# Performance work log

Measured on AMD Instinct MI355X. Metric: run time of the kernel, lower is better.

Reference implementation:

```python
import jax, jax.numpy as jnp
import numpy as np

N = 50000      # nodes
E = 800000     # edges
F_IN = 512     # input feature dim
H1 = 8         # heads layer 1
F_HID = 8      # per-head hidden dim (concat -> 64)
H2 = 1         # heads layer 2
NLAB = 64      # output classes
LRELU_SLOPE = 0.2


def setup_inputs() -> dict:
    key = jax.random.key(0)
    ks = jax.random.split(key, 9)
    inputs = jax.random.normal(ks[0], (N, F_IN), jnp.float32)
    src = jax.random.randint(ks[1], (E,), 0, N, dtype=jnp.int32)
    dst = jax.random.randint(ks[2], (E,), 0, N, dtype=jnp.int32)
    s1 = 1.0 / np.sqrt(F_IN)
    s2 = 1.0 / np.sqrt(H1 * F_HID)
    W1 = jax.random.normal(ks[3], (H1, F_IN, F_HID), jnp.float32) * s1
    a1_src = jax.random.normal(ks[4], (H1, F_HID), jnp.float32) * 0.1
    a1_dst = jax.random.normal(ks[5], (H1, F_HID), jnp.float32) * 0.1
    W2 = jax.random.normal(ks[6], (H2, H1 * F_HID, NLAB), jnp.float32) * s2
    a2_src = jax.random.normal(ks[7], (H2, NLAB), jnp.float32) * 0.1
    a2_dst = jax.random.normal(ks[8], (H2, NLAB), jnp.float32) * 0.1
    return {"inputs": inputs, "W1": W1, "a1_src": a1_src, "a1_dst": a1_dst,
            "W2": W2, "a2_src": a2_src, "a2_dst": a2_dst, "src": src, "dst": dst}


def gat_layer(x, W, a_s, a_d, src, dst):
    # x: [N, F]; W: [H, F, O]; a_s/a_d: [H, O]
    Wh = jnp.einsum('nf,hfo->nho', x, W)                    # [N, H, O]
    es = jnp.einsum('nho,ho->nh', Wh, a_s)                  # [N, H]
    ed = jnp.einsum('nho,ho->nh', Wh, a_d)                  # [N, H]
    e = jax.nn.leaky_relu(es[src] + ed[dst], LRELU_SLOPE)   # [E, H]
    # neighborhood softmax over incoming edges of each dst node
    m = jax.lax.stop_gradient(jax.ops.segment_max(e, dst, num_segments=N))
    ex = jnp.exp(e - m[dst])                                # [E, H]
    den = jax.ops.segment_sum(ex, dst, num_segments=N)      # [N, H]
    alpha = ex / (den[dst] + 1e-10)                         # [E, H]
    msgs = alpha[:, :, None] * Wh[src]                      # [E, H, O]
    return jax.ops.segment_sum(msgs, dst, num_segments=N)   # [N, H, O]


def reference(inputs, W1, a1_src, a1_dst, W2, a2_src, a2_dst, src, dst):
    # eval mode: dropout rate 0, identity
    h = gat_layer(inputs, W1, a1_src, a1_dst, src, dst)     # [N, H1, F_HID]
    h = jax.nn.elu(h.reshape(N, H1 * F_HID))                # concat heads (reduction=False)
    o = gat_layer(h, W2, a2_src, a2_dst, src, dst)          # [N, H2, NLAB]
    o = o.mean(axis=1)                                      # average heads (reduction=True)
    return jax.nn.softmax(o, axis=-1)                       # [N, NLAB] (squeezed)
```

## Files before the change

### kernel.cpp

```cpp
#include <hip/hip_runtime.h>
#include <math.h>

#define N_NODES 50000
#define N_EDGES 800000
#define F_IN    512
#define H1      8
#define F_HID   8
#define C1      64
#define NLAB    64
#define SLOPE   0.2f
#define MAXDEG  64

#define NBIN    98
#define BINCAP  9216
#define NBLK_WT  128
#define NBLK_E   196
#define NBLK_G1  782

typedef __attribute__((ext_vector_type(8))) short short8;
typedef __attribute__((ext_vector_type(4))) float f32x4;

__device__ __forceinline__ float bf_lo(unsigned u) { return __uint_as_float(u << 16); }
__device__ __forceinline__ float bf_hi(unsigned u) { return __uint_as_float(u & 0xFFFF0000u); }
__device__ __forceinline__ unsigned short f2bf(float x) {
    unsigned bits = __float_as_uint(x);
    return (unsigned short)((bits + 0x7FFF + ((bits >> 16) & 1)) >> 16);
}

__global__ void k_prep(const float* __restrict__ W1, unsigned short* __restrict__ Bh,
                       unsigned short* __restrict__ Bl) {
    int i = blockIdx.x * 256 + threadIdx.x;
    int c = i >> 9, f = i & 511;
    float v = W1[(c >> 3) * (F_IN * F_HID) + f * F_HID + (c & 7)];
    unsigned bits = __float_as_uint(v);
    float r = v - __uint_as_float(bits & 0xFFFF0000u);
    Bh[i] = (unsigned short)(bits >> 16);
    Bl[i] = (unsigned short)(__float_as_uint(r) >> 16);
}

__launch_bounds__(256, 4)
__global__ void k_gemm1b(const float* __restrict__ X, const unsigned short* __restrict__ Bh,
                         const unsigned short* __restrict__ Bl, const float* __restrict__ a_s,
                         const float* __restrict__ a_d, float* __restrict__ es1,
                         unsigned short* __restrict__ wh1, float* __restrict__ ed,
                         const int* __restrict__ src, const int* __restrict__ dst,
                         int2* __restrict__ ebuf, int* __restrict__ gctr) {
    __shared__ unsigned short sBh[64][136];
    __shared__ unsigned short sBl[64][136];

    const int b = blockIdx.x;
    const int t = threadIdx.x;
    if (b < NBLK_E) {
        int* hist = (int*)&sBh[0][0];
        int* cur  = hist + 128;
        if (t < NBIN) hist[t] = 0;
        __syncthreads();
        int4 dv[4], sv[4];
        const int e0 = b * 4096 + t * 4;
        #pragma unroll
        for (int i = 0; i < 4; i++) {
            int e = e0 + i * 1024;
            if (e < N_EDGES) {
                dv[i] = *(const int4*)(dst + e);
                sv[i] = *(const int4*)(src + e);
                atomicAdd(&hist[dv[i].x >> 9], 1);
                atomicAdd(&hist[dv[i].y >> 9], 1);
                atomicAdd(&hist[dv[i].z >> 9], 1);
                atomicAdd(&hist[dv[i].w >> 9], 1);
            }
        }
        __syncthreads();
        if (t < NBIN) cur[t] = atomicAdd(&gctr[t], hist[t]);
        __syncthreads();
        #pragma unroll
        for (int i = 0; i < 4; i++) {
            int e = e0 + i * 1024;
            if (e < N_EDGES) {
                int d, s, sl;
                d = dv[i].x; s = sv[i].x; sl = atomicAdd(&cur[d >> 9], 1);
                ebuf[(size_t)(d >> 9) * BINCAP + min(sl, BINCAP - 1)] = make_int2(d, s);
                d = dv[i].y; s = sv[i].y; sl = atomicAdd(&cur[d >> 9], 1);
                ebuf[(size_t)(d >> 9) * BINCAP + min(sl, BINCAP - 1)] = make_int2(d, s);
                d = dv[i].z; s = sv[i].z; sl = atomicAdd(&cur[d >> 9], 1);
                ebuf[(size_t)(d >> 9) * BINCAP + min(sl, BINCAP - 1)] = make_int2(d, s);
                d = dv[i].w; s = sv[i].w; sl = atomicAdd(&cur[d >> 9], 1);
                ebuf[(size_t)(d >> 9) * BINCAP + min(sl, BINCAP - 1)] = make_int2(d, s);
            }
        }
        return;
    }

    const int lane = t & 63, w = t >> 6;
    const int r0 = (b - NBLK_E) * 64 + w * 16;
    const int m = lane & 15, quad = lane >> 4;
    int row = r0 + m; if (row >= N_NODES) row = N_NODES - 1;
    const float* xrow = X + (size_t)row * F_IN + quad * 8;

    const int sc = t >> 2;
    const int sp = t & 3;

    f32x4 acc[4] = {};
    float4 pxa[4], pxb[4];
    #pragma unroll
    for (int i = 0; i < 4; i++) {
        pxa[i] = *(const float4*)(xrow + i * 32);
        pxb[i] = *(const float4*)(xrow + i * 32 + 4);
    }

    for (int chunk = 0; chunk < 4; chunk++) {
        const int k0 = chunk * 128;
        if (chunk) __syncthreads();
        #pragma unroll
        for (int i = 0; i < 4; i++) {
            *(short8*)(&sBh[sc][sp * 32 + i * 8]) =
                *(const short8*)(Bh + sc * F_IN + k0 + sp * 32 + i * 8);
            *(short8*)(&sBl[sc][sp * 32 + i * 8]) =
                *(const short8*)(Bl + sc * F_IN + k0 + sp * 32 + i * 8);
        }
        __syncthreads();
        #pragma unroll
        for (int i = 0; i < 4; i++) {
            float xs[8] = {pxa[i].x, pxa[i].y, pxa[i].z, pxa[i].w,
                           pxb[i].x, pxb[i].y, pxb[i].z, pxb[i].w};
            if (chunk < 3) {
                const int ktn = k0 + 128 + i * 32;
                pxa[i] = *(const float4*)(xrow + ktn);
                pxb[i] = *(const float4*)(xrow + ktn + 4);
            }
            short8 ah, al;
            #pragma unroll
            for (int j = 0; j < 8; j++) {
                unsigned bits = __float_as_uint(xs[j]);
                float rr = xs[j] - __uint_as_float(bits & 0xFFFF0000u);
                ah[j] = (short)(bits >> 16);
                al[j] = (short)(__float_as_uint(rr) >> 16);
            }
            #pragma unroll
            for (int s = 0; s < 4; s++) {
                short8 bh = *(const short8*)(&sBh[s * 16 + m][i * 32 + quad * 8]);
                short8 bl = *(const short8*)(&sBl[s * 16 + m][i * 32 + quad * 8]);
                acc[s] = __builtin_amdgcn_mfma_f32_16x16x32_bf16(al, bh, acc[s], 0, 0, 0);
                acc[s] = __builtin_amdgcn_mfma_f32_16x16x32_bf16(ah, bl, acc[s], 0, 0, 0);
                acc[s] = __builtin_amdgcn_mfma_f32_16x16x32_bf16(ah, bh, acc[s], 0, 0, 0);
            }
        }
    }
    __syncthreads();
    unsigned short* sWh = &sBh[0][0] + w * 1024;
    #pragma unroll
    for (int s = 0; s < 4; s++)
        #pragma unroll
        for (int reg = 0; reg < 4; reg++)
            sWh[(quad * 4 + reg) * 64 + s * 16 + m] = f2bf(acc[s][reg]);
    __syncthreads();
    const int rr = lane & 15, p = lane >> 4;
    const int n = r0 + rr;
    if (n >= N_NODES) return;
    float es2v[2], edv[2];
    #pragma unroll
    for (int hh = 0; hh < 2; hh++) {
        int h = 2 * p + hh;
        float s = 0.f, dsum = 0.f;
        #pragma unroll
        for (int j = 0; j < 8; j++) {
            float v = __uint_as_float((unsigned)sWh[rr * 64 + h * 8 + j] << 16);
            s += v * a_s[h * 8 + j];
            dsum += v * a_d[h * 8 + j];
        }
        es2v[hh] = s; edv[hh] = dsum;
    }
    *(float2*)(es1 + n * 8 + 2 * p) = make_float2(es2v[0], es2v[1]);
    *(short8*)(wh1 + (size_t)n * 64 + p * 16)     = *(const short8*)(sWh + rr * 64 + p * 16);
    *(short8*)(wh1 + (size_t)n * 64 + p * 16 + 8) = *(const short8*)(sWh + rr * 64 + p * 16 + 8);
    *(float2*)(ed + n * 8 + 2 * p) = make_float2(edv[0], edv[1]);
}

__global__ void k_csr(const int2* __restrict__ ebuf, const int* __restrict__ gctr,
                      int* __restrict__ deg, int* __restrict__ colPad) {
    __shared__ int cnt[512];
    const int b = blockIdx.x, t = threadIdx.x;
    const int lo = b << 9;
    const int cnum = min(gctr[b], BINCAP);
    for (int i = t; i < 512; i += 256) cnt[i] = 0;
    __syncthreads();
    const int2* eb2 = ebuf + (size_t)b * BINCAP;
    for (int i = t; i < cnum; i += 256) {
        int2 e = eb2[i];
        int sl = atomicAdd(&cnt[e.x - lo], 1);
        colPad[(e.x << 6) | min(sl, MAXDEG - 1)] = e.y;
    }
    __syncthreads();
    for (int i = t; i < 512; i += 256) {
        int n = lo + i;
        if (n < N_NODES) deg[n] = min(cnt[i], MAXDEG);
    }
}

__launch_bounds__(256)
__global__ void k_agg1g2(const float* __restrict__ es1, const unsigned short* __restrict__ wh1,
                         const float* __restrict__ ed,
                         const int* __restrict__ deg, const int* __restrict__ colPad,
                         const float* __restrict__ W2, const float* __restrict__ a2s,
                         const float* __restrict__ a2d,
                         float* __restrict__ es2, unsigned short* __restrict__ wh2,
                         float* __restrict__ ed2) {
    __shared__ float Ws[64 * 64];
    __shared__ float hs[32][64];
    __shared__ int scol[32][68];
    const int t = threadIdx.x;
    #pragma unroll
    for (int i = 0; i < 4; i++) {
        int flat = i * 256 + t;
        *(float4*)(Ws + flat * 4) = *(const float4*)(W2 + flat * 4);
    }
    const int n0 = blockIdx.x * 32;
    for (int i = t; i < 512; i += 256) {
        size_t gi = (size_t)n0 * 16 + i;
        int4 v = (gi < (size_t)N_NODES * 16) ? ((const int4*)colPad)[gi]
                                             : make_int4(0, 0, 0, 0);
        *(int4*)&scol[i >> 4][(i & 15) * 4] = v;
    }
    __syncthreads();

    const int nl = t >> 3, q = t & 7;
    const int n = n0 + nl;
    float o[8] = {};
    if (n < N_NODES) {
        const int d = deg[n];
        const float edq = ed[n * 8 + q];
        float den = 0.f;
        float acc[8] = {};
        #pragma unroll 4
        for (int e = 0; e < d; ++e) {
            int sv = scol[nl][e];
            float x = es1[sv * 8 + q] + edq;
            uint4 u = *(const uint4*)(wh1 + (size_t)sv * 64 + q * 8);
            x = x > 0.f ? x : SLOPE * x;
            float wg = __expf(x);
            den += wg;
            acc[0] += wg * bf_lo(u.x); acc[1] += wg * bf_hi(u.x);
            acc[2] += wg * bf_lo(u.y); acc[3] += wg * bf_hi(u.y);
            acc[4] += wg * bf_lo(u.z); acc[5] += wg * bf_hi(u.z);
            acc[6] += wg * bf_lo(u.w); acc[7] += wg * bf_hi(u.w);
        }
        float inv = 1.f / (den + 1e-10f);
        #pragma unroll
        for (int j = 0; j < 8; j++) {
            float v = acc[j] * inv;
            o[j] = v > 0.f ? v : expm1f(v);
        }
    }
    float4* hp = (float4*)(&hs[nl][q * 8]);
    hp[0] = make_float4(o[0], o[1], o[2], o[3]);
    hp[1] = make_float4(o[4], o[5], o[6], o[7]);
    __syncthreads();

    const int wv = t >> 6, lane = t & 63;
    float as = a2s[lane], ad = a2d[lane];
    #pragma unroll
    for (int j = 0; j < 8; j++) {
        int nn = n0 + wv * 8 + j;
        if (nn >= N_NODES) break;
        float acc = 0.f;
        #pragma unroll
        for (int k = 0; k < 64; k++) acc += hs[wv * 8 + j][k] * Ws[k * 64 + lane];
        wh2[(size_t)nn * 64 + lane] = f2bf(acc);
        float s = acc * as;
        float dd = acc * ad;
        #pragma unroll
        for (int off = 1; off < 64; off <<= 1) {
            s += __shfl_xor(s, off);
            dd += __shfl_xor(dd, off);
        }
        if (lane == 0) { es2[nn] = s; ed2[nn] = dd; }
    }
}

__launch_bounds__(256)
__global__ void k_agg2(const float* __restrict__ es2, const unsigned short* __restrict__ wh2,
                       const float* __restrict__ ed2,
                       const int* __restrict__ deg, const int* __restrict__ colPad,
                       float* __restrict__ out) {
    __shared__ int scol[32][68];
    const int t = threadIdx.x;
    const int n0 = blockIdx.x * 32;
    for (int i = t; i < 512; i += 256) {
        size_t gi = (size_t)n0 * 16 + i;
        int4 v = (gi < (size_t)N_NODES * 16) ? ((const int4*)colPad)[gi]
                                             : make_int4(0, 0, 0, 0);
        *(int4*)&scol[i >> 4][(i & 15) * 4] = v;
    }
    __syncthreads();

    const int nl = t >> 3, q = t & 7;
    const int n = n0 + nl;
    if (n >= N_NODES) return;
    const int d = deg[n];
    const float edn = ed2[n];

    float den = 0.f;
    float acc[8] = {};
    #pragma unroll 4
    for (int e = 0; e < d; ++e) {
        int sv = scol[nl][e];
        float x = es2[sv] + edn;
        uint4 u = *(const uint4*)(wh2 + (size_t)sv * 64 + q * 8);
        x = x > 0.f ? x : SLOPE * x;
        float wg = __expf(x);
        den += wg;
        acc[0] += wg * bf_lo(u.x); acc[1] += wg * bf_hi(u.x);
        acc[2] += wg * bf_lo(u.y); acc[3] += wg * bf_hi(u.y);
        acc[4] += wg * bf_lo(u.z); acc[5] += wg * bf_hi(u.z);
        acc[6] += wg * bf_lo(u.w); acc[7] += wg * bf_hi(u.w);
    }
    float inv = 1.f / (den + 1e-10f);
    float o[8];
    #pragma unroll
    for (int j = 0; j < 8; j++) o[j] = acc[j] * inv;
    float mx = o[0];
    #pragma unroll
    for (int j = 1; j < 8; j++) mx = fmaxf(mx, o[j]);
    mx = fmaxf(mx, __shfl_xor(mx, 1));
    mx = fmaxf(mx, __shfl_xor(mx, 2));
    mx = fmaxf(mx, __shfl_xor(mx, 4));
    float e8[8], sm = 0.f;
    #pragma unroll
    for (int j = 0; j < 8; j++) { e8[j] = __expf(o[j] - mx); sm += e8[j]; }
    sm += __shfl_xor(sm, 1);
    sm += __shfl_xor(sm, 2);
    sm += __shfl_xor(sm, 4);
    float inv2 = 1.f / sm;
    float4* op = (float4*)(out + (size_t)n * 64 + q * 8);
    op[0] = make_float4(e8[0] * inv2, e8[1] * inv2, e8[2] * inv2, e8[3] * inv2);
    op[1] = make_float4(e8[4] * inv2, e8[5] * inv2, e8[6] * inv2, e8[7] * inv2);
}

extern "C" void kernel_launch(void* const* d_in, const int* in_sizes, int n_in,
                              void* d_out, int out_size, void* d_ws, size_t ws_size,
                              hipStream_t stream) {
    const float* X   = (const float*)d_in[0];
    const float* W1  = (const float*)d_in[1];
    const float* a1s = (const float*)d_in[2];
    const float* a1d = (const float*)d_in[3];
    const float* W2  = (const float*)d_in[4];
    const float* a2s = (const float*)d_in[5];
    const float* a2d = (const float*)d_in[6];
    const int*   src = (const int*)d_in[7];
    const int*   dst = (const int*)d_in[8];
    float* out = (float*)d_out;

    char* w = (char*)d_ws;
    size_t off = 0;
    auto alloc = [&](size_t bytes) {
        void* p = w + off;
        off += (bytes + 255) & ~(size_t)255;
        return p;
    };
    unsigned short* Bh   = (unsigned short*)alloc((size_t)C1 * F_IN * 2);
    unsigned short* Bl   = (unsigned short*)alloc((size_t)C1 * F_IN * 2);
    float*          es1  = (float*)alloc((size_t)N_NODES * 8 * 4);
    unsigned short* wh1  = (unsigned short*)alloc((size_t)N_NODES * 64 * 2);
    float*          es2  = (float*)alloc((size_t)N_NODES * 4);
    unsigned short* wh2  = (unsigned short*)alloc((size_t)N_NODES * 64 * 2);
    float*          ed1  = (float*)alloc((size_t)N_NODES * 8 * 4);
    float*          ed2  = (float*)alloc((size_t)N_NODES * 4);
    int*            deg  = (int*)alloc((size_t)N_NODES * 4);
    int*            colPad = (int*)alloc((size_t)N_NODES * MAXDEG * 4);
    int2*           ebuf = (int2*)alloc((size_t)NBIN * BINCAP * 8);
    int*            gctr = (int*)alloc((size_t)NBIN * 4);

    hipMemsetAsync(gctr, 0, NBIN * 4, stream);

    k_prep<<<NBLK_WT, 256, 0, stream>>>(W1, Bh, Bl);
    k_gemm1b<<<NBLK_E + NBLK_G1, 256, 0, stream>>>(X, Bh, Bl, a1s, a1d, es1, wh1, ed1,
                                                   src, dst, ebuf, gctr);
    k_csr<<<NBIN, 256, 0, stream>>>(ebuf, gctr, deg, colPad);
    k_agg1g2<<<(N_NODES + 31) / 32, 256, 0, stream>>>(es1, wh1, ed1, deg, colPad,
                                                      W2, a2s, a2d, es2, wh2, ed2);
    k_agg2<<<(N_NODES + 31) / 32, 256, 0, stream>>>(es2, wh2, ed2, deg, colPad, out);
}
```

Before: 257.8 us.

## Fuse all GAT phases into one cooperative persistent kernel with grid syncs

```diff
diff --git a/kernel.cpp b/kernel.cpp
--- a/kernel.cpp
+++ b/kernel.cpp
@@ -1,5 +1,8 @@
 #include <hip/hip_runtime.h>
+#include <hip/hip_cooperative_groups.h>
 #include <math.h>
+
+namespace cg = cooperative_groups;
 
 #define N_NODES 50000
 #define N_EDGES 800000
@@ -16,6 +19,8 @@
 #define NBLK_WT  128
 #define NBLK_E   196
 #define NBLK_G1  782
+#define NCHUNK  1563
+#define SMEMSZ  34816
 
 typedef __attribute__((ext_vector_type(8))) short short8;
 typedef __attribute__((ext_vector_type(4))) float f32x4;
@@ -27,9 +32,11 @@
     return (unsigned short)((bits + 0x7FFF + ((bits >> 16) & 1)) >> 16);
 }
 
-__global__ void k_prep(const float* __restrict__ W1, unsigned short* __restrict__ Bh,
-                       unsigned short* __restrict__ Bl) {
-    int i = blockIdx.x * 256 + threadIdx.x;
+
+__device__ __forceinline__ void ph_w1split(int task, int t, const float* __restrict__ W1,
+                                           unsigned short* __restrict__ Bh,
+                                           unsigned short* __restrict__ Bl) {
+    int i = task * 256 + t;
     int c = i >> 9, f = i & 511;
     float v = W1[(c >> 3) * (F_IN * F_HID) + f * F_HID + (c & 7)];
     unsigned bits = __float_as_uint(v);
@@ -38,64 +45,80 @@
     Bl[i] = (unsigned short)(__float_as_uint(r) >> 16);
 }
 
-__launch_bounds__(256, 4)
-__global__ void k_gemm1b(const float* __restrict__ X, const unsigned short* __restrict__ Bh,
-                         const unsigned short* __restrict__ Bl, const float* __restrict__ a_s,
-                         const float* __restrict__ a_d, float* __restrict__ es1,
-                         unsigned short* __restrict__ wh1, float* __restrict__ ed,
-                         const int* __restrict__ src, const int* __restrict__ dst,
-                         int2* __restrict__ ebuf, int* __restrict__ gctr) {
-    __shared__ unsigned short sBh[64][136];
-    __shared__ unsigned short sBl[64][136];
-
-    const int b = blockIdx.x;
-    const int t = threadIdx.x;
-    if (b < NBLK_E) {
-        int* hist = (int*)&sBh[0][0];
-        int* cur  = hist + 128;
-        if (t < NBIN) hist[t] = 0;
-        __syncthreads();
-        int4 dv[4], sv[4];
-        const int e0 = b * 4096 + t * 4;
-        #pragma unroll
-        for (int i = 0; i < 4; i++) {
-            int e = e0 + i * 1024;
-            if (e < N_EDGES) {
-                dv[i] = *(const int4*)(dst + e);
-                sv[i] = *(const int4*)(src + e);
-                atomicAdd(&hist[dv[i].x >> 9], 1);
-                atomicAdd(&hist[dv[i].y >> 9], 1);
-                atomicAdd(&hist[dv[i].z >> 9], 1);
-                atomicAdd(&hist[dv[i].w >> 9], 1);
-            }
-        }
-        __syncthreads();
-        if (t < NBIN) cur[t] = atomicAdd(&gctr[t], hist[t]);
-        __syncthreads();
-        #pragma unroll
-        for (int i = 0; i < 4; i++) {
-            int e = e0 + i * 1024;
-            if (e < N_EDGES) {
-                int d, s, sl;
-                d = dv[i].x; s = sv[i].x; sl = atomicAdd(&cur[d >> 9], 1);
-                ebuf[(size_t)(d >> 9) * BINCAP + min(sl, BINCAP - 1)] = make_int2(d, s);
-                d = dv[i].y; s = sv[i].y; sl = atomicAdd(&cur[d >> 9], 1);
-                ebuf[(size_t)(d >> 9) * BINCAP + min(sl, BINCAP - 1)] = make_int2(d, s);
-                d = dv[i].z; s = sv[i].z; sl = atomicAdd(&cur[d >> 9], 1);
-                ebuf[(size_t)(d >> 9) * BINCAP + min(sl, BINCAP - 1)] = make_int2(d, s);
-                d = dv[i].w; s = sv[i].w; sl = atomicAdd(&cur[d >> 9], 1);
-                ebuf[(size_t)(d >> 9) * BINCAP + min(sl, BINCAP - 1)] = make_int2(d, s);
-            }
-        }
-        return;
-    }
-
+__device__ __forceinline__ void ph_bin(int task, int t, char* smem,
+                                       const int* __restrict__ src, const int* __restrict__ dst,
+                                       int2* __restrict__ ebuf, int* __restrict__ gctr) {
+    int* hist = (int*)smem;
+    int* cur  = hist + 128;
+    if (t < NBIN) hist[t] = 0;
+    __syncthreads();
+    int4 dv[4], sv[4];
+    const int e0 = task * 4096 + t * 4;
+    #pragma unroll
+    for (int i = 0; i < 4; i++) {
+        int e = e0 + i * 1024;
+        if (e < N_EDGES) {
+            dv[i] = *(const int4*)(dst + e);
+            sv[i] = *(const int4*)(src + e);
+            atomicAdd(&hist[dv[i].x >> 9], 1);
+            atomicAdd(&hist[dv[i].y >> 9], 1);
+            atomicAdd(&hist[dv[i].z >> 9], 1);
+            atomicAdd(&hist[dv[i].w >> 9], 1);
+        }
+    }
+    __syncthreads();
+    if (t < NBIN) cur[t] = atomicAdd(&gctr[t], hist[t]);
+    __syncthreads();
+    #pragma unroll
+    for (int i = 0; i < 4; i++) {
+        int e = e0 + i * 1024;
+        if (e < N_EDGES) {
+            int d, s, sl;
+            d = dv[i].x; s = sv[i].x; sl = atomicAdd(&cur[d >> 9], 1);
+            ebuf[(size_t)(d >> 9) * BINCAP + min(sl, BINCAP - 1)] = make_int2(d, s);
+            d = dv[i].y; s = sv[i].y; sl = atomicAdd(&cur[d >> 9], 1);
+            ebuf[(size_t)(d >> 9) * BINCAP + min(sl, BINCAP - 1)] = make_int2(d, s);
+            d = dv[i].z; s = sv[i].z; sl = atomicAdd(&cur[d >> 9], 1);
+            ebuf[(size_t)(d >> 9) * BINCAP + min(sl, BINCAP - 1)] = make_int2(d, s);
+            d = dv[i].w; s = sv[i].w; sl = atomicAdd(&cur[d >> 9], 1);
+            ebuf[(size_t)(d >> 9) * BINCAP + min(sl, BINCAP - 1)] = make_int2(d, s);
+        }
+    }
+}
+
+__device__ __forceinline__ void ph_csr(int b, int t, char* smem,
+                                       const int2* __restrict__ ebuf, const int* __restrict__ gctr,
+                                       int* __restrict__ deg, int* __restrict__ colPad) {
+    int* cnt = (int*)smem;
+    const int lo = b << 9;
+    const int cnum = min(gctr[b], BINCAP);
+    for (int i = t; i < 512; i += 256) cnt[i] = 0;
+    __syncthreads();
+    const int2* eb2 = ebuf + (size_t)b * BINCAP;
+    for (int i = t; i < cnum; i += 256) {
+        int2 e = eb2[i];
+        int sl = atomicAdd(&cnt[e.x - lo], 1);
+        colPad[(e.x << 6) | min(sl, MAXDEG - 1)] = e.y;
+    }
+    __syncthreads();
+    for (int i = t; i < 512; i += 256) {
+        int n = lo + i;
+        if (n < N_NODES) deg[n] = min(cnt[i], MAXDEG);
+    }
+}
+
+__device__ __forceinline__ void ph_gemm1(int g, int t, char* smem,
+        const float* __restrict__ X, const unsigned short* __restrict__ Bh,
+        const unsigned short* __restrict__ Bl, const float* __restrict__ a1s,
+        const float* __restrict__ a1d, float* __restrict__ es1,
+        unsigned short* __restrict__ wh1, float* __restrict__ ed1) {
+    unsigned short (*sBh)[136] = (unsigned short(*)[136])smem;
+    unsigned short (*sBl)[136] = (unsigned short(*)[136])(smem + 17408);
     const int lane = t & 63, w = t >> 6;
-    const int r0 = (b - NBLK_E) * 64 + w * 16;
+    const int r0 = g * 64 + w * 16;
     const int m = lane & 15, quad = lane >> 4;
     int row = r0 + m; if (row >= N_NODES) row = N_NODES - 1;
     const float* xrow = X + (size_t)row * F_IN + quad * 8;
-
     const int sc = t >> 2;
     const int sp = t & 3;
 
@@ -106,7 +129,6 @@
         pxa[i] = *(const float4*)(xrow + i * 32);
         pxb[i] = *(const float4*)(xrow + i * 32 + 4);
     }
-
     for (int chunk = 0; chunk < 4; chunk++) {
         const int k0 = chunk * 128;
         if (chunk) __syncthreads();
@@ -146,7 +168,7 @@
         }
     }
     __syncthreads();
-    unsigned short* sWh = &sBh[0][0] + w * 1024;
+    unsigned short* sWh = (unsigned short*)smem + w * 1024;
     #pragma unroll
     for (int s = 0; s < 4; s++)
         #pragma unroll
@@ -164,56 +186,24 @@
         #pragma unroll
         for (int j = 0; j < 8; j++) {
             float v = __uint_as_float((unsigned)sWh[rr * 64 + h * 8 + j] << 16);
-            s += v * a_s[h * 8 + j];
-            dsum += v * a_d[h * 8 + j];
+            s += v * a1s[h * 8 + j];
+            dsum += v * a1d[h * 8 + j];
         }
         es2v[hh] = s; edv[hh] = dsum;
     }
     *(float2*)(es1 + n * 8 + 2 * p) = make_float2(es2v[0], es2v[1]);
     *(short8*)(wh1 + (size_t)n * 64 + p * 16)     = *(const short8*)(sWh + rr * 64 + p * 16);
     *(short8*)(wh1 + (size_t)n * 64 + p * 16 + 8) = *(const short8*)(sWh + rr * 64 + p * 16 + 8);
-    *(float2*)(ed + n * 8 + 2 * p) = make_float2(edv[0], edv[1]);
-}
-
-__global__ void k_csr(const int2* __restrict__ ebuf, const int* __restrict__ gctr,
-                      int* __restrict__ deg, int* __restrict__ colPad) {
-    __shared__ int cnt[512];
-    const int b = blockIdx.x, t = threadIdx.x;
-    const int lo = b << 9;
-    const int cnum = min(gctr[b], BINCAP);
-    for (int i = t; i < 512; i += 256) cnt[i] = 0;
-    __syncthreads();
-    const int2* eb2 = ebuf + (size_t)b * BINCAP;
-    for (int i = t; i < cnum; i += 256) {
-        int2 e = eb2[i];
-        int sl = atomicAdd(&cnt[e.x - lo], 1);
-        colPad[(e.x << 6) | min(sl, MAXDEG - 1)] = e.y;
-    }
-    __syncthreads();
-    for (int i = t; i < 512; i += 256) {
-        int n = lo + i;
-        if (n < N_NODES) deg[n] = min(cnt[i], MAXDEG);
-    }
-}
-
-__launch_bounds__(256)
-__global__ void k_agg1g2(const float* __restrict__ es1, const unsigned short* __restrict__ wh1,
-                         const float* __restrict__ ed,
-                         const int* __restrict__ deg, const int* __restrict__ colPad,
-                         const float* __restrict__ W2, const float* __restrict__ a2s,
-                         const float* __restrict__ a2d,
-                         float* __restrict__ es2, unsigned short* __restrict__ wh2,
-                         float* __restrict__ ed2) {
-    __shared__ float Ws[64 * 64];
-    __shared__ float hs[32][64];
-    __shared__ int scol[32][68];
-    const int t = threadIdx.x;
-    #pragma unroll
-    for (int i = 0; i < 4; i++) {
-        int flat = i * 256 + t;
-        *(float4*)(Ws + flat * 4) = *(const float4*)(W2 + flat * 4);
-    }
-    const int n0 = blockIdx.x * 32;
+    *(float2*)(ed1 + n * 8 + 2 * p) = make_float2(edv[0], edv[1]);
+}
+
+__device__ __forceinline__ void ph_aggC(int n0, int t, const float* Ws, float (*hs)[64],
+        int (*scol)[68],
+        const float* __restrict__ es1, const unsigned short* __restrict__ wh1,
+        const float* __restrict__ ed1, const int* __restrict__ deg,
+        const int* __restrict__ colPad, const float* __restrict__ a2s,
+        const float* __restrict__ a2d, float* __restrict__ es2,
+        unsigned short* __restrict__ wh2, float* __restrict__ ed2) {
     for (int i = t; i < 512; i += 256) {
         size_t gi = (size_t)n0 * 16 + i;
         int4 v = (gi < (size_t)N_NODES * 16) ? ((const int4*)colPad)[gi]
@@ -221,13 +211,12 @@
         *(int4*)&scol[i >> 4][(i & 15) * 4] = v;
     }
     __syncthreads();
-
     const int nl = t >> 3, q = t & 7;
     const int n = n0 + nl;
     float o[8] = {};
     if (n < N_NODES) {
         const int d = deg[n];
-        const float edq = ed[n * 8 + q];
+        const float edq = ed1[n * 8 + q];
         float den = 0.f;
         float acc[8] = {};
         #pragma unroll 4
@@ -254,19 +243,18 @@
     hp[0] = make_float4(o[0], o[1], o[2], o[3]);
     hp[1] = make_float4(o[4], o[5], o[6], o[7]);
     __syncthreads();
-
     const int wv = t >> 6, lane = t & 63;
-    float as = a2s[lane], ad = a2d[lane];
+    const float as = a2s[lane], ad = a2d[lane];
     #pragma unroll
     for (int j = 0; j < 8; j++) {
         int nn = n0 + wv * 8 + j;
         if (nn >= N_NODES) break;
-        float acc = 0.f;
-        #pragma unroll
-        for (int k = 0; k < 64; k++) acc += hs[wv * 8 + j][k] * Ws[k * 64 + lane];
-        wh2[(size_t)nn * 64 + lane] = f2bf(acc);
-        float s = acc * as;
-        float dd = acc * ad;
+        float accv = 0.f;
+        #pragma unroll
+        for (int k = 0; k < 64; k++) accv += hs[wv * 8 + j][k] * Ws[k * 64 + lane];
+        wh2[(size_t)nn * 64 + lane] = f2bf(accv);
+        float s = accv * as;
+        float dd = accv * ad;
         #pragma unroll
         for (int off = 1; off < 64; off <<= 1) {
             s += __shfl_xor(s, off);
@@ -274,16 +262,13 @@
         }
         if (lane == 0) { es2[nn] = s; ed2[nn] = dd; }
     }
-}
-
-__launch_bounds__(256)
-__global__ void k_agg2(const float* __restrict__ es2, const unsigned short* __restrict__ wh2,
-                       const float* __restrict__ ed2,
-                       const int* __restrict__ deg, const int* __restrict__ colPad,
-                       float* __restrict__ out) {
-    __shared__ int scol[32][68];
-    const int t = threadIdx.x;
-    const int n0 = blockIdx.x * 32;
+    __syncthreads();
+}
+
+__device__ __forceinline__ void ph_aggD(int n0, int t, int (*scol)[68],
+        const float* __restrict__ es2, const unsigned short* __restrict__ wh2,
+        const float* __restrict__ ed2, const int* __restrict__ deg,
+        const int* __restrict__ colPad, float* __restrict__ out) {
     for (int i = t; i < 512; i += 256) {
         size_t gi = (size_t)n0 * 16 + i;
         int4 v = (gi < (size_t)N_NODES * 16) ? ((const int4*)colPad)[gi]
@@ -291,48 +276,169 @@
         *(int4*)&scol[i >> 4][(i & 15) * 4] = v;
     }
     __syncthreads();
-
     const int nl = t >> 3, q = t & 7;
     const int n = n0 + nl;
-    if (n >= N_NODES) return;
-    const int d = deg[n];
-    const float edn = ed2[n];
-
-    float den = 0.f;
-    float acc[8] = {};
-    #pragma unroll 4
-    for (int e = 0; e < d; ++e) {
-        int sv = scol[nl][e];
-        float x = es2[sv] + edn;
-        uint4 u = *(const uint4*)(wh2 + (size_t)sv * 64 + q * 8);
-        x = x > 0.f ? x : SLOPE * x;
-        float wg = __expf(x);
-        den += wg;
-        acc[0] += wg * bf_lo(u.x); acc[1] += wg * bf_hi(u.x);
-        acc[2] += wg * bf_lo(u.y); acc[3] += wg * bf_hi(u.y);
-        acc[4] += wg * bf_lo(u.z); acc[5] += wg * bf_hi(u.z);
-        acc[6] += wg * bf_lo(u.w); acc[7] += wg * bf_hi(u.w);
-    }
-    float inv = 1.f / (den + 1e-10f);
-    float o[8];
-    #pragma unroll
-    for (int j = 0; j < 8; j++) o[j] = acc[j] * inv;
-    float mx = o[0];
-    #pragma unroll
-    for (int j = 1; j < 8; j++) mx = fmaxf(mx, o[j]);
-    mx = fmaxf(mx, __shfl_xor(mx, 1));
-    mx = fmaxf(mx, __shfl_xor(mx, 2));
-    mx = fmaxf(mx, __shfl_xor(mx, 4));
-    float e8[8], sm = 0.f;
-    #pragma unroll
-    for (int j = 0; j < 8; j++) { e8[j] = __expf(o[j] - mx); sm += e8[j]; }
-    sm += __shfl_xor(sm, 1);
-    sm += __shfl_xor(sm, 2);
-    sm += __shfl_xor(sm, 4);
-    float inv2 = 1.f / sm;
-    float4* op = (float4*)(out + (size_t)n * 64 + q * 8);
-    op[0] = make_float4(e8[0] * inv2, e8[1] * inv2, e8[2] * inv2, e8[3] * inv2);
-    op[1] = make_float4(e8[4] * inv2, e8[5] * inv2, e8[6] * inv2, e8[7] * inv2);
+    if (n < N_NODES) {
+        const int d = deg[n];
+        const float edn = ed2[n];
+        float den = 0.f;
+        float acc[8] = {};
+        #pragma unroll 4
+        for (int e = 0; e < d; ++e) {
+            int sv = scol[nl][e];
+            float x = es2[sv] + edn;
+            uint4 u = *(const uint4*)(wh2 + (size_t)sv * 64 + q * 8);
+            x = x > 0.f ? x : SLOPE * x;
+            float wg = __expf(x);
+            den += wg;
+            acc[0] += wg * bf_lo(u.x); acc[1] += wg * bf_hi(u.x);
+            acc[2] += wg * bf_lo(u.y); acc[3] += wg * bf_hi(u.y);
+            acc[4] += wg * bf_lo(u.z); acc[5] += wg * bf_hi(u.z);
+            acc[6] += wg * bf_lo(u.w); acc[7] += wg * bf_hi(u.w);
+        }
+        float inv = 1.f / (den + 1e-10f);
+        float o[8];
+        #pragma unroll
+        for (int j = 0; j < 8; j++) o[j] = acc[j] * inv;
+        float mx = o[0];
+        #pragma unroll
+        for (int j = 1; j < 8; j++) mx = fmaxf(mx, o[j]);
+        mx = fmaxf(mx, __shfl_xor(mx, 1));
+        mx = fmaxf(mx, __shfl_xor(mx, 2));
+        mx = fmaxf(mx, __shfl_xor(mx, 4));
+        float e8[8], sm = 0.f;
+        #pragma unroll
+        for (int j = 0; j < 8; j++) { e8[j] = __expf(o[j] - mx); sm += e8[j]; }
+        sm += __shfl_xor(sm, 1);
+        sm += __shfl_xor(sm, 2);
+        sm += __shfl_xor(sm, 4);
+        float inv2 = 1.f / sm;
+        float4* op = (float4*)(out + (size_t)n * 64 + q * 8);
+        op[0] = make_float4(e8[0] * inv2, e8[1] * inv2, e8[2] * inv2, e8[3] * inv2);
+        op[1] = make_float4(e8[4] * inv2, e8[5] * inv2, e8[6] * inv2, e8[7] * inv2);
+    }
+    __syncthreads();
+}
+
+__launch_bounds__(256, 4)
+__global__ void k_mega(const float* __restrict__ X, const float* __restrict__ W1,
+                       const float* __restrict__ a1s, const float* __restrict__ a1d,
+                       const float* __restrict__ W2, const float* __restrict__ a2s,
+                       const float* __restrict__ a2d,
+                       const int* __restrict__ src, const int* __restrict__ dst,
+                       unsigned short* __restrict__ Bh, unsigned short* __restrict__ Bl,
+                       float* __restrict__ es1, unsigned short* __restrict__ wh1,
+                       float* __restrict__ ed1,
+                       float* __restrict__ es2, unsigned short* __restrict__ wh2,
+                       float* __restrict__ ed2,
+                       int* __restrict__ deg, int* __restrict__ colPad,
+                       int2* __restrict__ ebuf, int* __restrict__ gctr,
+                       float* __restrict__ out) {
+    __shared__ __align__(16) char smem[SMEMSZ];
+    __shared__ int sChunk;
+    cg::grid_group grid = cg::this_grid();
+    const int t = threadIdx.x;
+    const int nblk = gridDim.x;
+    int* wctrC = gctr + NBIN;
+    int* wctrD = gctr + NBIN + 1;
+
+    for (int task = blockIdx.x; task < NBLK_WT + NBLK_E; task += nblk) {
+        if (task < NBLK_WT) ph_w1split(task, t, W1, Bh, Bl);
+        else ph_bin(task - NBLK_WT, t, smem, src, dst, ebuf, gctr);
+        __syncthreads();
+    }
+    __threadfence();
+    grid.sync();
+
+    for (int task = blockIdx.x; task < NBIN + NBLK_G1; task += nblk) {
+        if (task < NBIN) ph_csr(task, t, smem, ebuf, gctr, deg, colPad);
+        else ph_gemm1(task - NBIN, t, smem, X, Bh, Bl, a1s, a1d, es1, wh1, ed1);
+        __syncthreads();
+    }
+    __threadfence();
+    grid.sync();
+
+    {
+        float* Ws = (float*)smem;
+        float (*hs)[64] = (float(*)[64])(smem + 16384);
+        int (*scol)[68] = (int(*)[68])(smem + 24576);
+        #pragma unroll
+        for (int i = 0; i < 4; i++) {
+            int flat = i * 256 + t;
+            *(float4*)(Ws + flat * 4) = *(const float4*)(W2 + flat * 4);
+        }
+        while (true) {
+            if (t == 0) sChunk = atomicAdd(wctrC, 1);
+            __syncthreads();
+            const int c = sChunk;
+            if (c >= NCHUNK) break;
+            ph_aggC(c * 32, t, Ws, hs, scol, es1, wh1, ed1, deg, colPad,
+                    a2s, a2d, es2, wh2, ed2);
+        }
+    }
+    __threadfence();
+    grid.sync();
+
+    {
+        int (*scol)[68] = (int(*)[68])smem;
+        while (true) {
+            if (t == 0) sChunk = atomicAdd(wctrD, 1);
+            __syncthreads();
+            const int c = sChunk;
+            if (c >= NCHUNK) break;
+            ph_aggD(c * 32, t, scol, es2, wh2, ed2, deg, colPad, out);
+        }
+    }
+}
+
+__global__ void k_phA(const float* __restrict__ W1, unsigned short* __restrict__ Bh,
+                      unsigned short* __restrict__ Bl, const int* __restrict__ src,
+                      const int* __restrict__ dst, int2* __restrict__ ebuf,
+                      int* __restrict__ gctr) {
+    __shared__ __align__(16) char smem[1024];
+    if (blockIdx.x < NBLK_WT) ph_w1split(blockIdx.x, threadIdx.x, W1, Bh, Bl);
+    else ph_bin(blockIdx.x - NBLK_WT, threadIdx.x, smem, src, dst, ebuf, gctr);
+}
+
+__launch_bounds__(256, 4)
+__global__ void k_phB(const float* __restrict__ X, const unsigned short* __restrict__ Bh,
+                      const unsigned short* __restrict__ Bl, const float* __restrict__ a1s,
+                      const float* __restrict__ a1d, float* __restrict__ es1,
+                      unsigned short* __restrict__ wh1, float* __restrict__ ed1,
+                      const int2* __restrict__ ebuf, const int* __restrict__ gctr,
+                      int* __restrict__ deg, int* __restrict__ colPad) {
+    __shared__ __align__(16) char smem[SMEMSZ];
+    if (blockIdx.x < NBIN) ph_csr(blockIdx.x, threadIdx.x, smem, ebuf, gctr, deg, colPad);
+    else ph_gemm1(blockIdx.x - NBIN, threadIdx.x, smem, X, Bh, Bl, a1s, a1d, es1, wh1, ed1);
+}
+
+__launch_bounds__(256)
+__global__ void k_phC(const float* __restrict__ es1, const unsigned short* __restrict__ wh1,
+                      const float* __restrict__ ed1, const int* __restrict__ deg,
+                      const int* __restrict__ colPad, const float* __restrict__ W2,
+                      const float* __restrict__ a2s, const float* __restrict__ a2d,
+                      float* __restrict__ es2, unsigned short* __restrict__ wh2,
+                      float* __restrict__ ed2) {
+    __shared__ __align__(16) char smem[33280];
+    float* Ws = (float*)smem;
+    float (*hs)[64] = (float(*)[64])(smem + 16384);
+    int (*scol)[68] = (int(*)[68])(smem + 24576);
+    const int t = threadIdx.x;
+    #pragma unroll
+    for (int i = 0; i < 4; i++) {
+        int flat = i * 256 + t;
+        *(float4*)(Ws + flat * 4) = *(const float4*)(W2 + flat * 4);
+    }
+    ph_aggC(blockIdx.x * 32, t, Ws, hs, scol, es1, wh1, ed1, deg, colPad,
+            a2s, a2d, es2, wh2, ed2);
+}
+
+__launch_bounds__(256)
+__global__ void k_phD(const float* __restrict__ es2, const unsigned short* __restrict__ wh2,
+                      const float* __restrict__ ed2, const int* __restrict__ deg,
+                      const int* __restrict__ colPad, float* __restrict__ out) {
+    __shared__ __align__(16) char smem[8704];
+    ph_aggD(blockIdx.x * 32, threadIdx.x, (int(*)[68])smem, es2, wh2, ed2, deg, colPad, out);
 }
 
 extern "C" void kernel_launch(void* const* d_in, const int* in_sizes, int n_in,
@@ -367,15 +473,42 @@
     int*            deg  = (int*)alloc((size_t)N_NODES * 4);
     int*            colPad = (int*)alloc((size_t)N_NODES * MAXDEG * 4);
     int2*           ebuf = (int2*)alloc((size_t)NBIN * BINCAP * 8);
-    int*            gctr = (int*)alloc((size_t)NBIN * 4);
-
-    hipMemsetAsync(gctr, 0, NBIN * 4, stream);
-
-    k_prep<<<NBLK_WT, 256, 0, stream>>>(W1, Bh, Bl);
-    k_gemm1b<<<NBLK_E + NBLK_G1, 256, 0, stream>>>(X, Bh, Bl, a1s, a1d, es1, wh1, ed1,
-                                                   src, dst, ebuf, gctr);
-    k_csr<<<NBIN, 256, 0, stream>>>(ebuf, gctr, deg, colPad);
-    k_agg1g2<<<(N_NODES + 31) / 32, 256, 0, stream>>>(es1, wh1, ed1, deg, colPad,
-                                                      W2, a2s, a2d, es2, wh2, ed2);
-    k_agg2<<<(N_NODES + 31) / 32, 256, 0, stream>>>(es2, wh2, ed2, deg, colPad, out);
-}
+    int*            gctr = (int*)alloc((size_t)(NBIN + 2) * 4);
+
+    hipMemsetAsync(gctr, 0, (NBIN + 2) * 4, stream);
+
+    static int coopGrid = -2;
+    if (coopGrid == -2) {
+        int nb = 0;
+        hipError_t qe = hipOccupancyMaxActiveBlocksPerMultiprocessor(&nb, k_mega, 256, 0);
+        if (qe == hipSuccess && nb >= 1) {
+            if (nb > 4) nb = 4;
+            coopGrid = nb * 256;
+        } else {
+            coopGrid = 0;
+        }
+    }
+
+    bool launched = false;
+    if (coopGrid > 0) {
+        void* args[] = {
+            (void*)&X, (void*)&W1, (void*)&a1s, (void*)&a1d, (void*)&W2,
+            (void*)&a2s, (void*)&a2d, (void*)&src, (void*)&dst,
+            (void*)&Bh, (void*)&Bl, (void*)&es1, (void*)&wh1, (void*)&ed1,
+            (void*)&es2, (void*)&wh2, (void*)&ed2, (void*)&deg, (void*)&colPad,
+            (void*)&ebuf, (void*)&gctr, (void*)&out
+        };
+        hipError_t le = hipLaunchCooperativeKernel((const void*)k_mega, dim3(coopGrid),
+                                                   dim3(256), args, 0, stream);
+        if (le == hipSuccess) launched = true;
+        else coopGrid = 0;
+    }
+    if (!launched) {
+        k_phA<<<NBLK_WT + NBLK_E, 256, 0, stream>>>(W1, Bh, Bl, src, dst, ebuf, gctr);
+        k_phB<<<NBIN + NBLK_G1, 256, 0, stream>>>(X, Bh, Bl, a1s, a1d, es1, wh1, ed1,
+                                                  ebuf, gctr, deg, colPad);
+        k_phC<<<NCHUNK, 256, 0, stream>>>(es1, wh1, ed1, deg, colPad, W2, a2s, a2d,
+                                          es2, wh2, ed2);
+        k_phD<<<NCHUNK, 256, 0, stream>>>(es2, wh2, ed2, deg, colPad, out);
+    }
+}
```

Result: slower. 661.7 us (+156.7%).

## Merge weight prep with edge binning, co-schedule CSR build with GEMM1, and pack indices to 16-bit

Applied to the files above, without the earlier changes.

```diff
diff --git a/kernel.cpp b/kernel.cpp
--- a/kernel.cpp
+++ b/kernel.cpp
@@ -16,6 +16,7 @@
 #define NBLK_WT  128
 #define NBLK_E   196
 #define NBLK_G1  782
+#define NCHUNK  1563
 
 typedef __attribute__((ext_vector_type(8))) short short8;
 typedef __attribute__((ext_vector_type(4))) float f32x4;
@@ -27,75 +28,99 @@
     return (unsigned short)((bits + 0x7FFF + ((bits >> 16) & 1)) >> 16);
 }
 
-__global__ void k_prep(const float* __restrict__ W1, unsigned short* __restrict__ Bh,
-                       unsigned short* __restrict__ Bl) {
-    int i = blockIdx.x * 256 + threadIdx.x;
-    int c = i >> 9, f = i & 511;
-    float v = W1[(c >> 3) * (F_IN * F_HID) + f * F_HID + (c & 7)];
-    unsigned bits = __float_as_uint(v);
-    float r = v - __uint_as_float(bits & 0xFFFF0000u);
-    Bh[i] = (unsigned short)(bits >> 16);
-    Bl[i] = (unsigned short)(__float_as_uint(r) >> 16);
-}
-
-__launch_bounds__(256, 4)
-__global__ void k_gemm1b(const float* __restrict__ X, const unsigned short* __restrict__ Bh,
-                         const unsigned short* __restrict__ Bl, const float* __restrict__ a_s,
-                         const float* __restrict__ a_d, float* __restrict__ es1,
-                         unsigned short* __restrict__ wh1, float* __restrict__ ed,
-                         const int* __restrict__ src, const int* __restrict__ dst,
-                         int2* __restrict__ ebuf, int* __restrict__ gctr) {
-    __shared__ unsigned short sBh[64][136];
-    __shared__ unsigned short sBl[64][136];
-
+__global__ void k_prepbin(const float* __restrict__ W1, unsigned short* __restrict__ Bh,
+                          unsigned short* __restrict__ Bl,
+                          const int* __restrict__ src, const int* __restrict__ dst,
+                          unsigned* __restrict__ ebuf, int* __restrict__ gctr) {
     const int b = blockIdx.x;
     const int t = threadIdx.x;
-    if (b < NBLK_E) {
-        int* hist = (int*)&sBh[0][0];
-        int* cur  = hist + 128;
-        if (t < NBIN) hist[t] = 0;
+    if (b < NBLK_WT) {
+        int i = b * 256 + t;
+        int c = i >> 9, f = i & 511;
+        float v = W1[(c >> 3) * (F_IN * F_HID) + f * F_HID + (c & 7)];
+        unsigned bits = __float_as_uint(v);
+        float r = v - __uint_as_float(bits & 0xFFFF0000u);
+        Bh[i] = (unsigned short)(bits >> 16);
+        Bl[i] = (unsigned short)(__float_as_uint(r) >> 16);
+        return;
+    }
+    __shared__ int hist[NBIN];
+    __shared__ int cur[NBIN];
+    if (t < NBIN) hist[t] = 0;
+    __syncthreads();
+    int4 dv[4], sv[4];
+    const int e0 = (b - NBLK_WT) * 4096 + t * 4;
+    #pragma unroll
+    for (int i = 0; i < 4; i++) {
+        int e = e0 + i * 1024;
+        if (e < N_EDGES) {
+            dv[i] = *(const int4*)(dst + e);
+            sv[i] = *(const int4*)(src + e);
+            atomicAdd(&hist[dv[i].x >> 9], 1);
+            atomicAdd(&hist[dv[i].y >> 9], 1);
+            atomicAdd(&hist[dv[i].z >> 9], 1);
+            atomicAdd(&hist[dv[i].w >> 9], 1);
+        }
+    }
+    __syncthreads();
+    if (t < NBIN) cur[t] = atomicAdd(&gctr[t], hist[t]);
+    __syncthreads();
+    #pragma unroll
+    for (int i = 0; i < 4; i++) {
+        int e = e0 + i * 1024;
+        if (e < N_EDGES) {
+            int d, s, sl;
+            d = dv[i].x; s = sv[i].x; sl = atomicAdd(&cur[d >> 9], 1);
+            ebuf[(size_t)(d >> 9) * BINCAP + min(sl, BINCAP - 1)] = ((unsigned)(d & 511) << 16) | (unsigned)s;
+            d = dv[i].y; s = sv[i].y; sl = atomicAdd(&cur[d >> 9], 1);
+            ebuf[(size_t)(d >> 9) * BINCAP + min(sl, BINCAP - 1)] = ((unsigned)(d & 511) << 16) | (unsigned)s;
+            d = dv[i].z; s = sv[i].z; sl = atomicAdd(&cur[d >> 9], 1);
+            ebuf[(size_t)(d >> 9) * BINCAP + min(sl, BINCAP - 1)] = ((unsigned)(d & 511) << 16) | (unsigned)s;
+            d = dv[i].w; s = sv[i].w; sl = atomicAdd(&cur[d >> 9], 1);
+            ebuf[(size_t)(d >> 9) * BINCAP + min(sl, BINCAP - 1)] = ((unsigned)(d & 511) << 16) | (unsigned)s;
+        }
+    }
+}
+
+__launch_bounds__(256, 4)
+__global__ void k_g1csr(const float* __restrict__ X, const unsigned short* __restrict__ Bh,
+                        const unsigned short* __restrict__ Bl, const float* __restrict__ a1s,
+                        const float* __restrict__ a1d, float* __restrict__ es1,
+                        unsigned short* __restrict__ wh1, float* __restrict__ ed1,
+                        const unsigned* __restrict__ ebuf, const int* __restrict__ gctr,
+                        int* __restrict__ deg, unsigned short* __restrict__ colPad) {
+    __shared__ __align__(16) char smem[34816];
+    const int b = blockIdx.x;
+    const int t = threadIdx.x;
+
+    if (b < NBIN) {
+        int* cnt = (int*)smem;
+        const int lo = b << 9;
+        const int cnum = min(gctr[b], BINCAP);
+        for (int i = t; i < 512; i += 256) cnt[i] = 0;
         __syncthreads();
-        int4 dv[4], sv[4];
-        const int e0 = b * 4096 + t * 4;
-        #pragma unroll
-        for (int i = 0; i < 4; i++) {
-            int e = e0 + i * 1024;
-            if (e < N_EDGES) {
-                dv[i] = *(const int4*)(dst + e);
-                sv[i] = *(const int4*)(src + e);
-                atomicAdd(&hist[dv[i].x >> 9], 1);
-                atomicAdd(&hist[dv[i].y >> 9], 1);
-                atomicAdd(&hist[dv[i].z >> 9], 1);
-                atomicAdd(&hist[dv[i].w >> 9], 1);
-            }
+        const unsigned* eb2 = ebuf + (size_t)b * BINCAP;
+        for (int i = t; i < cnum; i += 256) {
+            unsigned e = eb2[i];
+            int dl = (int)(e >> 16);
+            int sl = atomicAdd(&cnt[dl], 1);
+            colPad[((size_t)(lo + dl) << 6) | min(sl, MAXDEG - 1)] = (unsigned short)(e & 0xFFFFu);
         }
         __syncthreads();
-        if (t < NBIN) cur[t] = atomicAdd(&gctr[t], hist[t]);
-        __syncthreads();
-        #pragma unroll
-        for (int i = 0; i < 4; i++) {
-            int e = e0 + i * 1024;
-            if (e < N_EDGES) {
-                int d, s, sl;
-                d = dv[i].x; s = sv[i].x; sl = atomicAdd(&cur[d >> 9], 1);
-                ebuf[(size_t)(d >> 9) * BINCAP + min(sl, BINCAP - 1)] = make_int2(d, s);
-                d = dv[i].y; s = sv[i].y; sl = atomicAdd(&cur[d >> 9], 1);
-                ebuf[(size_t)(d >> 9) * BINCAP + min(sl, BINCAP - 1)] = make_int2(d, s);
-                d = dv[i].z; s = sv[i].z; sl = atomicAdd(&cur[d >> 9], 1);
-                ebuf[(size_t)(d >> 9) * BINCAP + min(sl, BINCAP - 1)] = make_int2(d, s);
-                d = dv[i].w; s = sv[i].w; sl = atomicAdd(&cur[d >> 9], 1);
-                ebuf[(size_t)(d >> 9) * BINCAP + min(sl, BINCAP - 1)] = make_int2(d, s);
-            }
+        for (int i = t; i < 512; i += 256) {
+            int n = lo + i;
+            if (n < N_NODES) deg[n] = min(cnt[i], MAXDEG);
         }
         return;
     }
 
+    unsigned short (*sBh)[136] = (unsigned short(*)[136])smem;
+    unsigned short (*sBl)[136] = (unsigned short(*)[136])(smem + 17408);
     const int lane = t & 63, w = t >> 6;
-    const int r0 = (b - NBLK_E) * 64 + w * 16;
+    const int r0 = (b - NBIN) * 64 + w * 16;
     const int m = lane & 15, quad = lane >> 4;
     int row = r0 + m; if (row >= N_NODES) row = N_NODES - 1;
     const float* xrow = X + (size_t)row * F_IN + quad * 8;
-
     const int sc = t >> 2;
     const int sp = t & 3;
 
@@ -106,7 +131,6 @@
         pxa[i] = *(const float4*)(xrow + i * 32);
         pxb[i] = *(const float4*)(xrow + i * 32 + 4);
     }
-
     for (int chunk = 0; chunk < 4; chunk++) {
         const int k0 = chunk * 128;
         if (chunk) __syncthreads();
@@ -146,7 +170,7 @@
         }
     }
     __syncthreads();
-    unsigned short* sWh = &sBh[0][0] + w * 1024;
+    unsigned short* sWh = (unsigned short*)smem + w * 1024;
     #pragma unroll
     for (int s = 0; s < 4; s++)
         #pragma unroll
@@ -164,49 +188,28 @@
         #pragma unroll
         for (int j = 0; j < 8; j++) {
             float v = __uint_as_float((unsigned)sWh[rr * 64 + h * 8 + j] << 16);
-            s += v * a_s[h * 8 + j];
-            dsum += v * a_d[h * 8 + j];
+            s += v * a1s[h * 8 + j];
+            dsum += v * a1d[h * 8 + j];
         }
         es2v[hh] = s; edv[hh] = dsum;
     }
     *(float2*)(es1 + n * 8 + 2 * p) = make_float2(es2v[0], es2v[1]);
     *(short8*)(wh1 + (size_t)n * 64 + p * 16)     = *(const short8*)(sWh + rr * 64 + p * 16);
     *(short8*)(wh1 + (size_t)n * 64 + p * 16 + 8) = *(const short8*)(sWh + rr * 64 + p * 16 + 8);
-    *(float2*)(ed + n * 8 + 2 * p) = make_float2(edv[0], edv[1]);
-}
-
-__global__ void k_csr(const int2* __restrict__ ebuf, const int* __restrict__ gctr,
-                      int* __restrict__ deg, int* __restrict__ colPad) {
-    __shared__ int cnt[512];
-    const int b = blockIdx.x, t = threadIdx.x;
-    const int lo = b << 9;
-    const int cnum = min(gctr[b], BINCAP);
-    for (int i = t; i < 512; i += 256) cnt[i] = 0;
-    __syncthreads();
-    const int2* eb2 = ebuf + (size_t)b * BINCAP;
-    for (int i = t; i < cnum; i += 256) {
-        int2 e = eb2[i];
-        int sl = atomicAdd(&cnt[e.x - lo], 1);
-        colPad[(e.x << 6) | min(sl, MAXDEG - 1)] = e.y;
-    }
-    __syncthreads();
-    for (int i = t; i < 512; i += 256) {
-        int n = lo + i;
-        if (n < N_NODES) deg[n] = min(cnt[i], MAXDEG);
-    }
+    *(float2*)(ed1 + n * 8 + 2 * p) = make_float2(edv[0], edv[1]);
 }
 
 __launch_bounds__(256)
 __global__ void k_agg1g2(const float* __restrict__ es1, const unsigned short* __restrict__ wh1,
-                         const float* __restrict__ ed,
-                         const int* __restrict__ deg, const int* __restrict__ colPad,
+                         const float* __restrict__ ed1,
+                         const int* __restrict__ deg, const unsigned short* __restrict__ colPad,
                          const float* __restrict__ W2, const float* __restrict__ a2s,
                          const float* __restrict__ a2d,
                          float* __restrict__ es2, unsigned short* __restrict__ wh2,
                          float* __restrict__ ed2) {
     __shared__ float Ws[64 * 64];
     __shared__ float hs[32][64];
-    __shared__ int scol[32][68];
+    __shared__ unsigned short scol[32][72];
     const int t = threadIdx.x;
     #pragma unroll
     for (int i = 0; i < 4; i++) {
@@ -214,11 +217,11 @@
         *(float4*)(Ws + flat * 4) = *(const float4*)(W2 + flat * 4);
     }
     const int n0 = blockIdx.x * 32;
-    for (int i = t; i < 512; i += 256) {
-        size_t gi = (size_t)n0 * 16 + i;
-        int4 v = (gi < (size_t)N_NODES * 16) ? ((const int4*)colPad)[gi]
-                                             : make_int4(0, 0, 0, 0);
-        *(int4*)&scol[i >> 4][(i & 15) * 4] = v;
+    {
+        size_t gi = (size_t)n0 * 8 + t;
+        int4 v = (gi < (size_t)N_NODES * 8) ? ((const int4*)colPad)[gi]
+                                            : make_int4(0, 0, 0, 0);
+        *(int4*)&scol[t >> 3][(t & 7) * 8] = v;
     }
     __syncthreads();
 
@@ -227,7 +230,7 @@
     float o[8] = {};
     if (n < N_NODES) {
         const int d = deg[n];
-        const float edq = ed[n * 8 + q];
+        const float edq = ed1[n * 8 + q];
         float den = 0.f;
         float acc[8] = {};
         #pragma unroll 4
@@ -256,17 +259,17 @@
     __syncthreads();
 
     const int wv = t >> 6, lane = t & 63;
-    float as = a2s[lane], ad = a2d[lane];
+    const float as = a2s[lane], ad = a2d[lane];
     #pragma unroll
     for (int j = 0; j < 8; j++) {
         int nn = n0 + wv * 8 + j;
         if (nn >= N_NODES) break;
-        float acc = 0.f;
-        #pragma unroll
-        for (int k = 0; k < 64; k++) acc += hs[wv * 8 + j][k] * Ws[k * 64 + lane];
-        wh2[(size_t)nn * 64 + lane] = f2bf(acc);
-        float s = acc * as;
-        float dd = acc * ad;
+        float accv = 0.f;
+        #pragma unroll
+        for (int k = 0; k < 64; k++) accv += hs[wv * 8 + j][k] * Ws[k * 64 + lane];
+        wh2[(size_t)nn * 64 + lane] = f2bf(accv);
+        float s = accv * as;
+        float dd = accv * ad;
         #pragma unroll
         for (int off = 1; off < 64; off <<= 1) {
             s += __shfl_xor(s, off);
@@ -279,16 +282,16 @@
 __launch_bounds__(256)
 __global__ void k_agg2(const float* __restrict__ es2, const unsigned short* __restrict__ wh2,
                        const float* __restrict__ ed2,
-                       const int* __restrict__ deg, const int* __restrict__ colPad,
+                       const int* __restrict__ deg, const unsigned short* __restrict__ colPad,
                        float* __restrict__ out) {
-    __shared__ int scol[32][68];
+    __shared__ unsigned short scol[32][72];
     const int t = threadIdx.x;
     const int n0 = blockIdx.x * 32;
-    for (int i = t; i < 512; i += 256) {
-        size_t gi = (size_t)n0 * 16 + i;
-        int4 v = (gi < (size_t)N_NODES * 16) ? ((const int4*)colPad)[gi]
-                                             : make_int4(0, 0, 0, 0);
-        *(int4*)&scol[i >> 4][(i & 15) * 4] = v;
+    {
+        size_t gi = (size_t)n0 * 8 + t;
+        int4 v = (gi < (size_t)N_NODES * 8) ? ((const int4*)colPad)[gi]
+                                            : make_int4(0, 0, 0, 0);
+        *(int4*)&scol[t >> 3][(t & 7) * 8] = v;
     }
     __syncthreads();
 
@@ -365,17 +368,16 @@
     float*          ed1  = (float*)alloc((size_t)N_NODES * 8 * 4);
     float*          ed2  = (float*)alloc((size_t)N_NODES * 4);
     int*            deg  = (int*)alloc((size_t)N_NODES * 4);
-    int*            colPad = (int*)alloc((size_t)N_NODES * MAXDEG * 4);
-    int2*           ebuf = (int2*)alloc((size_t)NBIN * BINCAP * 8);
+    unsigned short* colPad = (unsigned short*)alloc((size_t)N_NODES * MAXDEG * 2);
+    unsigned*       ebuf = (unsigned*)alloc((size_t)NBIN * BINCAP * 4);
     int*            gctr = (int*)alloc((size_t)NBIN * 4);
 
     hipMemsetAsync(gctr, 0, NBIN * 4, stream);
 
-    k_prep<<<NBLK_WT, 256, 0, stream>>>(W1, Bh, Bl);
-    k_gemm1b<<<NBLK_E + NBLK_G1, 256, 0, stream>>>(X, Bh, Bl, a1s, a1d, es1, wh1, ed1,
-                                                   src, dst, ebuf, gctr);
-    k_csr<<<NBIN, 256, 0, stream>>>(ebuf, gctr, deg, colPad);
-    k_agg1g2<<<(N_NODES + 31) / 32, 256, 0, stream>>>(es1, wh1, ed1, deg, colPad,
-                                                      W2, a2s, a2d, es2, wh2, ed2);
-    k_agg2<<<(N_NODES + 31) / 32, 256, 0, stream>>>(es2, wh2, ed2, deg, colPad, out);
-}
+    k_prepbin<<<NBLK_WT + NBLK_E, 256, 0, stream>>>(W1, Bh, Bl, src, dst, ebuf, gctr);
+    k_g1csr<<<NBIN + NBLK_G1, 256, 0, stream>>>(X, Bh, Bl, a1s, a1d, es1, wh1, ed1,
+                                                ebuf, gctr, deg, colPad);
+    k_agg1g2<<<NCHUNK, 256, 0, stream>>>(es1, wh1, ed1, deg, colPad,
+                                         W2, a2s, a2d, es2, wh2, ed2);
+    k_agg2<<<NCHUNK, 256, 0, stream>>>(es2, wh2, ed2, deg, colPad, out);
+}
```

Measured after the change: 256.4 us. About the same (-0.5%).
